# Kernel tuning notes

Measured on AMD Instinct MI355X. Metric: run time of the kernel, lower is better.

Reference implementation:

```python
import jax, jax.numpy as jnp
import numpy as np

D_EMB = 2048
N_HEADS = 16
D_K = D_EMB // N_HEADS  # 128
MAX_LEN = 128           # must equal D_K for the (faithful) buggy mask broadcast
VOCAB = 30000
N_LAYERS = 6
BATCH = 8
SEQ = 128
D_FF = 4 * D_EMB


def _sinusoidal_pe(length, d):
    pos = jnp.arange(length, dtype=jnp.float32)[:, None]
    div = jnp.exp(-jnp.log(10000.0) * jnp.arange(0, d, 2, dtype=jnp.float32) / d)
    pe = jnp.zeros((length, d), dtype=jnp.float32)
    pe = pe.at[:, 0::2].set(jnp.sin(pos * div))
    pe = pe.at[:, 1::2].set(jnp.cos(pos * div))
    return pe


def _layernorm(x, g, b, eps=1e-5):
    m = jnp.mean(x, axis=-1, keepdims=True)
    v = jnp.var(x, axis=-1, keepdims=True)
    return g * (x - m) * jax.lax.rsqrt(v + eps) + b


def _attention(x, ctx, Wq, Wk, Wv, Wo, mask):
    # Faithful to source: reshape [B,L,H,dk] then swap LAST TWO axes -> [B,L,dk,H],
    # so scores are [B,L,dk,dk] (attention over the d_k axis, per token).
    B, L, D = x.shape
    split = lambda t: t.reshape(B, L, N_HEADS, D_K).swapaxes(-2, -1)  # [B,L,dk,H]
    Q = split(x @ Wq.T)
    K = split(ctx @ Wk.T)
    V = split(ctx @ Wv.T)
    qk = (Q @ K.swapaxes(-2, -1)) / np.sqrt(D_K)  # [B,L,dk,dk]
    if mask is not None:
        qk = qk + mask  # mask [L,L] broadcasts (L == dk == max_len)
    attn = jax.nn.softmax(qk, axis=-1) @ V        # [B,L,dk,H]
    concat = attn.swapaxes(-2, -1).reshape(B, L, D)
    return concat @ Wo.T


def _decoder(x, context, params):
    p = params
    L = x.shape[1]
    x = x + _sinusoidal_pe(L, D_EMB)
    mask = jnp.triu(jnp.full((L, L), -jnp.inf, dtype=x.dtype), k=1)
    for _ in range(N_LAYERS):  # weights are SHARED across layers (as in source)
        x = _layernorm(_attention(x, x, p['Wq1'], p['Wk1'], p['Wv1'], p['Wo1'], mask),
                       p['g1'], p['be1'])
        x = _layernorm(_attention(x, context, p['Wq2'], p['Wk2'], p['Wv2'], p['Wo2'], None),
                       p['g2'], p['be2'])
        h = jax.nn.relu(x @ p['W_ff1'].T + p['b_ff1']) @ p['W_ff2'].T + p['b_ff2']
        x = _layernorm(h, p['g3'], p['be3'])
    logits = (x @ p['W_lin'].T + p['b_lin']) / 1.0  # temperature = 1.0
    # Faithful to source: softmax over dim=1 (sequence axis), then take last batch element
    return jax.nn.softmax(logits, axis=1)[-1]  # [L, VOCAB]


def setup_inputs() -> dict:
    key = jax.random.key(0)
    ks = jax.random.split(key, 20)
    a = np.sqrt(3.0 / D_EMB)
    u = lambda k, sh: jax.random.uniform(k, sh, jnp.float32, -a, a)
    inp = {
        'x': jax.random.normal(ks[0], (BATCH, SEQ, D_EMB), jnp.float32),
        'context': jax.random.normal(ks[1], (BATCH, SEQ, D_EMB), jnp.float32),
        'Wq1': u(ks[2], (D_EMB, D_EMB)), 'Wk1': u(ks[3], (D_EMB, D_EMB)),
        'Wv1': u(ks[4], (D_EMB, D_EMB)), 'Wo1': u(ks[5], (D_EMB, D_EMB)),
        'Wq2': u(ks[6], (D_EMB, D_EMB)), 'Wk2': u(ks[7], (D_EMB, D_EMB)),
        'Wv2': u(ks[8], (D_EMB, D_EMB)), 'Wo2': u(ks[9], (D_EMB, D_EMB)),
        'W_ff1': u(ks[10], (D_FF, D_EMB)), 'b_ff1': jnp.zeros((D_FF,), jnp.float32),
        'W_ff2': jax.random.uniform(ks[11], (D_EMB, D_FF), jnp.float32, -np.sqrt(1.0 / D_FF), np.sqrt(1.0 / D_FF)),
        'b_ff2': jnp.zeros((D_EMB,), jnp.float32),
        'g1': jnp.ones((D_EMB,), jnp.float32), 'be1': jnp.zeros((D_EMB,), jnp.float32),
        'g2': jnp.ones((D_EMB,), jnp.float32), 'be2': jnp.zeros((D_EMB,), jnp.float32),
        'g3': jnp.ones((D_EMB,), jnp.float32), 'be3': jnp.zeros((D_EMB,), jnp.float32),
        'W_lin': u(ks[12], (VOCAB, D_EMB)), 'b_lin': jnp.zeros((VOCAB,), jnp.float32),
    }
    return inp


def reference(x, context, Wq1, Wk1, Wv1, Wo1, Wq2, Wk2, Wv2, Wo2,
              W_ff1, b_ff1, W_ff2, b_ff2, g1, be1, g2, be2, g3, be3,
              W_lin, b_lin):
    params = dict(Wq1=Wq1, Wk1=Wk1, Wv1=Wv1, Wo1=Wo1,
                  Wq2=Wq2, Wk2=Wk2, Wv2=Wv2, Wo2=Wo2,
                  W_ff1=W_ff1, b_ff1=b_ff1, W_ff2=W_ff2, b_ff2=b_ff2,
                  g1=g1, be1=be1, g2=g2, be2=be2, g3=g3, be3=be3,
                  W_lin=W_lin, b_lin=b_lin)
    return _decoder(x, context, params)
```

## Files before the change

kernel.cpp:

```cpp
#include <hip/hip_runtime.h>
#include <hip/hip_bf16.h>
#include <math.h>

#define D_EMB 2048
#define NH 16
#define DK 128
#define SEQN 128
#define DFF 8192
#define VOCAB 30000
#define NLAYERS 6
#define TOKF (SEQN * D_EMB)

typedef __attribute__((ext_vector_type(8))) short short8v;
typedef __attribute__((ext_vector_type(4))) float float4v;
typedef __hip_bfloat16 bf16;

#define GLOAD_LDS16(g, l)                                                      \
    __builtin_amdgcn_global_load_lds(                                          \
        (const __attribute__((address_space(1))) void*)(g),                    \
        (__attribute__((address_space(3))) void*)(l), 16, 0, 0)

struct CvtArgs {
    const float* src[8];
    bf16* dst[8];
};

__global__ __launch_bounds__(256) void cvt_kernel(CvtArgs args, int n4) {
    int i = blockIdx.x * 256 + threadIdx.x;
    if (i >= n4) return;
    const float4* s = (const float4*)args.src[blockIdx.z];
    float4 v = s[i];
    union { short4 s4; bf16 h[4]; } u;
    u.h[0] = __float2bfloat16(v.x);
    u.h[1] = __float2bfloat16(v.y);
    u.h[2] = __float2bfloat16(v.z);
    u.h[3] = __float2bfloat16(v.w);
    ((short4*)args.dst[blockIdx.z])[i] = u.s4;
}

__global__ __launch_bounds__(256) void add_pe_kernel(const float* __restrict__ x,
                                                     bf16* __restrict__ out) {
    int idx = blockIdx.x * 256 + threadIdx.x;
    int l = idx >> 11;
    int d = idx & 2047;
    float two_i = (float)(d & ~1);
    float div = __expf(-9.210340371976184f * two_i * (1.0f / 2048.0f));
    float ang = (float)l * div;
    float pe = (d & 1) ? cosf(ang) : sinf(ang);
    out[idx] = __float2bfloat16(x[(size_t)7 * SEQN * D_EMB + idx] + pe);
}

__global__ __launch_bounds__(256) void gemm_mfma_kernel(
    const bf16* __restrict__ A,
    const bf16* B0, const bf16* B1, const bf16* B2,
    const float* bias0, const float* bias1, const float* bias2,
    void* C0, void* C1, void* C2,
    int M, int N, int K, int relu, int out_bf16, int ksplit, int kslog)
{
    int z = blockIdx.z;
    int oi = z >> kslog;
    int kh = z & (ksplit - 1);
    int Klocal = K >> kslog;
    int kbase = kh * Klocal;

    const bf16* B    = (oi == 0) ? B0    : (oi == 1) ? B1    : B2;
    const float* bias = (oi == 0) ? bias0 : (oi == 1) ? bias1 : bias2;
    void* C          = (oi == 0) ? C0    : (oi == 1) ? C1    : C2;

    __shared__ __align__(16) bf16 As[2][64 * 128];
    __shared__ __align__(16) bf16 Bs[2][64 * 128];

    int tid = threadIdx.x;
    int w = tid >> 6;
    int lane = tid & 63;
    int m0 = blockIdx.x * 64;
    int n0 = blockIdx.y * 64;
    int wm = (w & 1) * 32;
    int wn = (w >> 1) * 32;
    int fcol = lane & 15;
    int fqu  = lane >> 4;
    int rr   = (w << 2) + (lane >> 4);
    int scol = lane & 15;

    float4v acc[2][2];
    acc[0][0] = (float4v)0.0f; acc[0][1] = (float4v)0.0f;
    acc[1][0] = (float4v)0.0f; acc[1][1] = (float4v)0.0f;

    auto stage = [&](int buf, int k0) {
        #pragma unroll
        for (int t = 0; t < 4; ++t) {
            int r = t * 16 + rr;
            int s = scol ^ (r & 15);
            GLOAD_LDS16(A + (size_t)(m0 + r) * K + kbase + k0 + s * 8,
                        (char*)As[buf] + (size_t)(t * 16 + (w << 2)) * 256);
            GLOAD_LDS16(B + (size_t)(n0 + r) * K + kbase + k0 + s * 8,
                        (char*)Bs[buf] + (size_t)(t * 16 + (w << 2)) * 256);
        }
    };

    int nk = Klocal >> 7;
    stage(0, 0);
    for (int i = 0; i < nk; ++i) {
        int cur = i & 1;
        if (i + 1 < nk) {
            stage(cur ^ 1, (i + 1) << 7);
            asm volatile("s_waitcnt vmcnt(8)" ::: "memory");
        } else {
            asm volatile("s_waitcnt vmcnt(0)" ::: "memory");
        }
        __builtin_amdgcn_s_barrier();
        asm volatile("" ::: "memory");

        #pragma unroll
        for (int kk = 0; kk < 4; ++kk) {
            short8v a[2], b[2];
            int slog = kk * 4 + fqu;
            #pragma unroll
            for (int fm = 0; fm < 2; ++fm) {
                int m = wm + fm * 16 + fcol;
                a[fm] = *(const short8v*)((const char*)As[cur] + m * 256 + ((slog ^ (m & 15)) << 4));
            }
            #pragma unroll
            for (int fn = 0; fn < 2; ++fn) {
                int n = wn + fn * 16 + fcol;
                b[fn] = *(const short8v*)((const char*)Bs[cur] + n * 256 + ((slog ^ (n & 15)) << 4));
            }
            #pragma unroll
            for (int fm = 0; fm < 2; ++fm)
                #pragma unroll
                for (int fn = 0; fn < 2; ++fn)
                    acc[fm][fn] = __builtin_amdgcn_mfma_f32_16x16x32_bf16(
                        a[fm], b[fn], acc[fm][fn], 0, 0, 0);
        }
        asm volatile("" ::: "memory");
        __builtin_amdgcn_s_barrier();
    }

    int rbase = fqu * 4;
    #pragma unroll
    for (int fm = 0; fm < 2; ++fm) {
        #pragma unroll
        for (int fn = 0; fn < 2; ++fn) {
            int n = n0 + wn + fn * 16 + fcol;
            #pragma unroll
            for (int r = 0; r < 4; ++r) {
                int m = m0 + wm + fm * 16 + rbase + r;
                float v = acc[fm][fn][r];
                if (out_bf16) {
                    v += bias ? bias[n] : 0.0f;
                    if (relu) v = fmaxf(v, 0.0f);
                    ((bf16*)C)[(size_t)m * N + n] = __float2bfloat16(v);
                } else {
                    ((float*)C)[(size_t)kh * M * N + (size_t)m * N + n] = v;
                }
            }
        }
    }
}

__global__ __launch_bounds__(256) void attn_token_kernel(
    const float* __restrict__ qp,
    const float* __restrict__ kp, const float* __restrict__ vp,
    const bf16* __restrict__ k16, const bf16* __restrict__ v16,
    bf16* __restrict__ O, int causal, int qparts, int kvparts)
{
    int l = blockIdx.x;
    int tid = threadIdx.x;
    int i = tid & 127;
    int half = tid >> 7;
    __shared__ float qs[D_EMB];
    __shared__ float ks[D_EMB];
    __shared__ float vs[D_EMB];
    __shared__ float m1s[128], l1s[128];
    __shared__ float acc1s[128][NH + 1];
    size_t base = (size_t)l * D_EMB;

    for (int d = tid; d < D_EMB; d += 256) {
        float q = 0.0f;
        for (int p = 0; p < qparts; ++p) q += qp[(size_t)p * TOKF + base + d];
        qs[d] = q;
        if (kvparts) {
            float kv = 0.0f, vv = 0.0f;
            for (int p = 0; p < kvparts; ++p) {
                kv += kp[(size_t)p * TOKF + base + d];
                vv += vp[(size_t)p * TOKF + base + d];
            }
            ks[d] = kv; vs[d] = vv;
        } else {
            ks[d] = (float)k16[base + d];
            vs[d] = (float)v16[base + d];
        }
    }
    __syncthreads();

    const float scale = 0.088388347648318447f;
    float qr[NH];
    #pragma unroll
    for (int h = 0; h < NH; ++h) qr[h] = qs[h * DK + i];

    int jmax = causal ? (i + 1) : DK;
    int j0 = half * 64;
    int j1 = (jmax < j0 + 64) ? jmax : (j0 + 64);

    float m = -INFINITY, lsum = 0.0f;
    float acc[NH];
    #pragma unroll
    for (int h = 0; h < NH; ++h) acc[h] = 0.0f;

    for (int j = j0; j < j1; ++j) {
        float s0 = 0.0f, s1 = 0.0f, s2 = 0.0f, s3 = 0.0f;
        #pragma unroll
        for (int h = 0; h < NH; h += 4) {
            s0 += qr[h + 0] * ks[(h + 0) * DK + j];
            s1 += qr[h + 1] * ks[(h + 1) * DK + j];
            s2 += qr[h + 2] * ks[(h + 2) * DK + j];
            s3 += qr[h + 3] * ks[(h + 3) * DK + j];
        }
        float s = ((s0 + s1) + (s2 + s3)) * scale;
        float nm = fmaxf(m, s);
        float f = __expf(m - nm);
        float p = __expf(s - nm);
        lsum = lsum * f + p;
        #pragma unroll
        for (int h = 0; h < NH; ++h) acc[h] = acc[h] * f + p * vs[h * DK + j];
        m = nm;
    }

    if (half) {
        m1s[i] = m; l1s[i] = lsum;
        #pragma unroll
        for (int h = 0; h < NH; ++h) acc1s[i][h] = acc[h];
    }
    __syncthreads();
    if (!half) {
        float m1 = m1s[i], l1 = l1s[i];
        float nm = fmaxf(m, m1);
        float f0 = __expf(m - nm);
        float f1 = __expf(m1 - nm);
        float rinv = 1.0f / (lsum * f0 + l1 * f1);
        #pragma unroll
        for (int h = 0; h < NH; ++h)
            O[base + h * DK + i] =
                __float2bfloat16((acc[h] * f0 + acc1s[i][h] * f1) * rinv);
    }
}

__global__ __launch_bounds__(256) void layernorm_kernel(
    const float* __restrict__ pa, int nparts,
    const float* __restrict__ addb,
    const float* __restrict__ g, const float* __restrict__ b,
    bf16* __restrict__ Y)
{
    int row = blockIdx.x;
    size_t base = (size_t)row * D_EMB;
    __shared__ float vs[D_EMB];
    __shared__ float buf[256];
    int tid = threadIdx.x;

    float s = 0.0f;
    for (int d = tid; d < D_EMB; d += 256) {
        float v = addb ? addb[d] : 0.0f;
        for (int p = 0; p < nparts; ++p) v += pa[(size_t)p * TOKF + base + d];
        vs[d] = v;
        s += v;
    }
    buf[tid] = s; __syncthreads();
    for (int off = 128; off; off >>= 1) {
        if (tid < off) buf[tid] += buf[tid + off];
        __syncthreads();
    }
    float mean = buf[0] * (1.0f / D_EMB);
    __syncthreads();

    float vsum = 0.0f;
    for (int d = tid; d < D_EMB; d += 256) {
        float t = vs[d] - mean;
        vsum += t * t;
    }
    buf[tid] = vsum; __syncthreads();
    for (int off = 128; off; off >>= 1) {
        if (tid < off) buf[tid] += buf[tid + off];
        __syncthreads();
    }
    float inv = rsqrtf(buf[0] * (1.0f / D_EMB) + 1e-5f);

    for (int d = tid; d < D_EMB; d += 256)
        Y[base + d] = __float2bfloat16(g[d] * (vs[d] - mean) * inv + b[d]);
}

__global__ __launch_bounds__(256) void logits_softmax_kernel(
    const bf16* __restrict__ X, const float* __restrict__ W,
    float* __restrict__ out)
{
    __shared__ __align__(16) bf16 As[128 * 128];
    __shared__ __align__(16) bf16 Bs[64 * 128];
    __shared__ float red[4][64];

    int tid = threadIdx.x;
    int w = tid >> 6;
    int lane = tid & 63;
    int fcol = lane & 15;
    int fqu  = lane >> 4;
    int n0 = blockIdx.x * 64;

    float4v acc[2][4];
    #pragma unroll
    for (int fm = 0; fm < 2; ++fm)
        #pragma unroll
        for (int fn = 0; fn < 4; ++fn) acc[fm][fn] = (float4v)0.0f;

    int brow = tid >> 2;
    int q    = tid & 3;
    int gn   = n0 + brow;

    for (int k0 = 0; k0 < D_EMB; k0 += 128) {
        #pragma unroll
        for (int t = 0; t < 8; ++t) {
            int r = t * 16 + (w << 2) + (lane >> 4);
            int s = (lane & 15) ^ (r & 15);
            GLOAD_LDS16(X + (size_t)r * D_EMB + k0 + s * 8,
                        (char*)As + (size_t)(t * 16 + (w << 2)) * 256);
        }
        #pragma unroll
        for (int j = 0; j < 4; ++j) {
            int sL = q * 4 + j;
            union { short8v v; bf16 h[8]; } u;
            if (gn < VOCAB) {
                const float* gp = W + (size_t)gn * D_EMB + k0 + sL * 8;
                float4 f0 = *(const float4*)gp;
                float4 f1 = *(const float4*)(gp + 4);
                u.h[0] = __float2bfloat16(f0.x); u.h[1] = __float2bfloat16(f0.y);
                u.h[2] = __float2bfloat16(f0.z); u.h[3] = __float2bfloat16(f0.w);
                u.h[4] = __float2bfloat16(f1.x); u.h[5] = __float2bfloat16(f1.y);
                u.h[6] = __float2bfloat16(f1.z); u.h[7] = __float2bfloat16(f1.w);
            } else {
                u.v = (short8v)0;
            }
            *(short8v*)((char*)Bs + brow * 256 + ((sL ^ (brow & 15)) << 4)) = u.v;
        }
        __syncthreads();

        #pragma unroll
        for (int kk = 0; kk < 4; ++kk) {
            int slog = kk * 4 + fqu;
            short8v a[2], b[4];
            #pragma unroll
            for (int fm = 0; fm < 2; ++fm) {
                int m = w * 32 + fm * 16 + fcol;
                a[fm] = *(const short8v*)((const char*)As + m * 256 + ((slog ^ (m & 15)) << 4));
            }
            #pragma unroll
            for (int fn = 0; fn < 4; ++fn) {
                int n = fn * 16 + fcol;
                b[fn] = *(const short8v*)((const char*)Bs + n * 256 + ((slog ^ (n & 15)) << 4));
            }
            #pragma unroll
            for (int fm = 0; fm < 2; ++fm)
                #pragma unroll
                for (int fn = 0; fn < 4; ++fn)
                    acc[fm][fn] = __builtin_amdgcn_mfma_f32_16x16x32_bf16(
                        a[fm], b[fn], acc[fm][fn], 0, 0, 0);
        }
        __syncthreads();
    }

    float cmax[4];
    #pragma unroll
    for (int fn = 0; fn < 4; ++fn) {
        float m = -INFINITY;
        #pragma unroll
        for (int fm = 0; fm < 2; ++fm)
            #pragma unroll
            for (int r = 0; r < 4; ++r) m = fmaxf(m, acc[fm][fn][r]);
        m = fmaxf(m, __shfl_xor(m, 16));
        m = fmaxf(m, __shfl_xor(m, 32));
        cmax[fn] = m;
    }
    if (lane < 16) {
        #pragma unroll
        for (int fn = 0; fn < 4; ++fn) red[w][fn * 16 + lane] = cmax[fn];
    }
    __syncthreads();
    #pragma unroll
    for (int fn = 0; fn < 4; ++fn) {
        float m = red[0][fn * 16 + fcol];
        m = fmaxf(m, red[1][fn * 16 + fcol]);
        m = fmaxf(m, red[2][fn * 16 + fcol]);
        m = fmaxf(m, red[3][fn * 16 + fcol]);
        cmax[fn] = m;
    }
    __syncthreads();

    float csum[4];
    #pragma unroll
    for (int fn = 0; fn < 4; ++fn) {
        float s = 0.0f;
        #pragma unroll
        for (int fm = 0; fm < 2; ++fm)
            #pragma unroll
            for (int r = 0; r < 4; ++r) {
                float e = __expf(acc[fm][fn][r] - cmax[fn]);
                acc[fm][fn][r] = e;
                s += e;
            }
        s += __shfl_xor(s, 16);
        s += __shfl_xor(s, 32);
        csum[fn] = s;
    }
    if (lane < 16) {
        #pragma unroll
        for (int fn = 0; fn < 4; ++fn) red[w][fn * 16 + lane] = csum[fn];
    }
    __syncthreads();
    #pragma unroll
    for (int fn = 0; fn < 4; ++fn) {
        float s = red[0][fn * 16 + fcol] + red[1][fn * 16 + fcol]
                + red[2][fn * 16 + fcol] + red[3][fn * 16 + fcol];
        float rinv = 1.0f / s;
        int c = n0 + fn * 16 + fcol;
        if (c < VOCAB) {
            #pragma unroll
            for (int fm = 0; fm < 2; ++fm)
                #pragma unroll
                for (int r = 0; r < 4; ++r) {
                    int rw = w * 32 + fm * 16 + fqu * 4 + r;
                    out[(size_t)rw * VOCAB + c] = acc[fm][fn][r] * rinv;
                }
        }
    }
}

static inline void launch_gemm(const bf16* A,
                               const bf16* B0, const bf16* B1, const bf16* B2,
                               const float* bias0, const float* bias1, const float* bias2,
                               void* C0, void* C1, void* C2,
                               int M, int N, int K, int relu, int out_bf16,
                               int nout, int ksplit, int kslog, hipStream_t s)
{
    dim3 grid(M / 64, N / 64, nout * ksplit);
    hipLaunchKernelGGL(gemm_mfma_kernel, grid, dim3(256), 0, s,
                       A, B0, B1, B2, bias0, bias1, bias2, C0, C1, C2,
                       M, N, K, relu, out_bf16, ksplit, kslog);
}

extern "C" void kernel_launch(void* const* d_in, const int* in_sizes, int n_in,
                              void* d_out, int out_size, void* d_ws, size_t ws_size,
                              hipStream_t stream)
{
    const float* x_in   = (const float*)d_in[0];
    const float* ctx_in = (const float*)d_in[1];
    const float* Wq1 = (const float*)d_in[2];
    const float* Wk1 = (const float*)d_in[3];
    const float* Wv1 = (const float*)d_in[4];
    const float* Wo1 = (const float*)d_in[5];
    const float* Wq2 = (const float*)d_in[6];
    const float* Wk2 = (const float*)d_in[7];
    const float* Wv2 = (const float*)d_in[8];
    const float* Wo2 = (const float*)d_in[9];
    const float* W_ff1 = (const float*)d_in[10];
    const float* b_ff1 = (const float*)d_in[11];
    const float* W_ff2 = (const float*)d_in[12];
    const float* b_ff2 = (const float*)d_in[13];
    const float* g1  = (const float*)d_in[14];
    const float* be1 = (const float*)d_in[15];
    const float* g2  = (const float*)d_in[16];
    const float* be2 = (const float*)d_in[17];
    const float* g3  = (const float*)d_in[18];
    const float* be3 = (const float*)d_in[19];
    const float* W_lin = (const float*)d_in[20];
    float* out = (float*)d_out;

    const size_t W2 = (size_t)D_EMB * D_EMB;
    const size_t WF = (size_t)DFF * D_EMB;

    char* p = (char*)d_ws;
    bf16* wq1 = (bf16*)p; p += W2 * 2;
    bf16* wk1 = (bf16*)p; p += W2 * 2;
    bf16* wv1 = (bf16*)p; p += W2 * 2;
    bf16* wo1 = (bf16*)p; p += W2 * 2;
    bf16* wq2 = (bf16*)p; p += W2 * 2;
    bf16* wk2 = (bf16*)p; p += W2 * 2;
    bf16* wv2 = (bf16*)p; p += W2 * 2;
    bf16* wo2 = (bf16*)p; p += W2 * 2;
    bf16* wff1 = (bf16*)p; p += WF * 2;
    bf16* wff2 = (bf16*)p; p += WF * 2;
    bf16* wctx = (bf16*)p; p += (size_t)TOKF * 2;
    bf16* X    = (bf16*)p; p += (size_t)TOKF * 2;
    bf16* Att  = (bf16*)p; p += (size_t)TOKF * 2;
    bf16* H    = (bf16*)p; p += (size_t)SEQN * DFF * 2;
    float* Qp  = (float*)p; p += (size_t)4 * TOKF * 4;
    float* Kp  = (float*)p; p += (size_t)4 * TOKF * 4;
    float* Vp  = (float*)p; p += (size_t)4 * TOKF * 4;
    float* X2p = (float*)p; p += (size_t)8 * TOKF * 4;
    float* K2p = (float*)p; p += (size_t)2 * TOKF * 4;
    float* V2p = (float*)p; p += (size_t)2 * TOKF * 4;

    const float* ctx7 = ctx_in + (size_t)7 * SEQN * D_EMB;

    {
        CvtArgs a = {};
        a.src[0] = Wq1; a.dst[0] = wq1;  a.src[1] = Wk1; a.dst[1] = wk1;
        a.src[2] = Wv1; a.dst[2] = wv1;  a.src[3] = Wo1; a.dst[3] = wo1;
        a.src[4] = Wq2; a.dst[4] = wq2;  a.src[5] = Wk2; a.dst[5] = wk2;
        a.src[6] = Wv2; a.dst[6] = wv2;  a.src[7] = Wo2; a.dst[7] = wo2;
        int n4 = (int)(W2 / 4);
        hipLaunchKernelGGL(cvt_kernel, dim3((n4 + 255) / 256, 1, 8), dim3(256), 0,
                           stream, a, n4);
    }
    {
        CvtArgs a = {};
        a.src[0] = W_ff1; a.dst[0] = wff1;
        a.src[1] = W_ff2; a.dst[1] = wff2;
        int n4 = (int)(WF / 4);
        hipLaunchKernelGGL(cvt_kernel, dim3((n4 + 255) / 256, 1, 2), dim3(256), 0,
                           stream, a, n4);
    }
    {
        CvtArgs a = {};
        a.src[0] = ctx7; a.dst[0] = wctx;
        int n4 = TOKF / 4;
        hipLaunchKernelGGL(cvt_kernel, dim3((n4 + 255) / 256, 1, 1), dim3(256), 0,
                           stream, a, n4);
    }

    hipLaunchKernelGGL(add_pe_kernel, dim3((SEQN * D_EMB) / 256), dim3(256), 0,
                       stream, x_in, X);

    launch_gemm(wctx, wk2, wv2, wv2, nullptr, nullptr, nullptr,
                K2p, V2p, V2p, SEQN, D_EMB, D_EMB, 0, 0, 2, 2, 1, stream);

    for (int layer = 0; layer < NLAYERS; ++layer) {
        launch_gemm(X, wq1, wk1, wv1, nullptr, nullptr, nullptr,
                    Qp, Kp, Vp, SEQN, D_EMB, D_EMB, 0, 0, 3, 4, 2, stream);
        hipLaunchKernelGGL(attn_token_kernel, dim3(SEQN), dim3(256), 0, stream,
                           Qp, Kp, Vp,
                           (const bf16*)nullptr, (const bf16*)nullptr,
                           Att, 1, 4, 4);
        launch_gemm(Att, wo1, wo1, wo1, nullptr, nullptr, nullptr,
                    X2p, X2p, X2p, SEQN, D_EMB, D_EMB, 0, 0, 1, 4, 2, stream);
        hipLaunchKernelGGL(layernorm_kernel, dim3(SEQN), dim3(256), 0, stream,
                           X2p, 4, (const float*)nullptr, g1, be1, X);

        launch_gemm(X, wq2, wq2, wq2, nullptr, nullptr, nullptr,
                    Qp, Qp, Qp, SEQN, D_EMB, D_EMB, 0, 0, 1, 4, 2, stream);
        hipLaunchKernelGGL(attn_token_kernel, dim3(SEQN), dim3(256), 0, stream,
                           Qp, K2p, V2p,
                           (const bf16*)nullptr, (const bf16*)nullptr,
                           Att, 0, 4, 2);
        launch_gemm(Att, wo2, wo2, wo2, nullptr, nullptr, nullptr,
                    X2p, X2p, X2p, SEQN, D_EMB, D_EMB, 0, 0, 1, 4, 2, stream);
        hipLaunchKernelGGL(layernorm_kernel, dim3(SEQN), dim3(256), 0, stream,
                           X2p, 4, (const float*)nullptr, g2, be2, X);

        launch_gemm(X, wff1, wff1, wff1, b_ff1, b_ff1, b_ff1,
                    H, H, H, SEQN, DFF, D_EMB, 1, 1, 1, 1, 0, stream);
        launch_gemm(H, wff2, wff2, wff2, nullptr, nullptr, nullptr,
                    X2p, X2p, X2p, SEQN, D_EMB, DFF, 0, 0, 1, 8, 3, stream);
        hipLaunchKernelGGL(layernorm_kernel, dim3(SEQN), dim3(256), 0, stream,
                           X2p, 8, b_ff2, g3, be3, X);
    }

    hipLaunchKernelGGL(logits_softmax_kernel, dim3((VOCAB + 63) / 64), dim3(256),
                       0, stream, X, W_lin, out);
}
```

Before: 1.595 ms.

## Fix GEMM K-slices at 512 with four-stage prefetch, XCD swizzle, and vectorized helpers

The GEMM now always splits K into 512-wide slices and issues all four 128-wide chunks of a slice up front into four LDS buffers, waiting on each with staged vmcnt counts, which removes the loop and its per-iteration barriers. Workgroup IDs are remapped so consecutive tiles spread across the eight XCDs. FF1 becomes a split-K GEMM into fp32 partials followed by a separate bias+ReLU reduction kernel. Attention and layernorm move to float4 loads and a 4-wide online-softmax step. The cost is more fp32 partial traffic and reduction work (FF2 now has 16 partials), doubled LDS per block that may lower occupancy, and an extra kernel launch per layer.

```diff
diff --git a/kernel.cpp b/kernel.cpp
--- a/kernel.cpp
+++ b/kernel.cpp
@@ -19,6 +19,13 @@
     __builtin_amdgcn_global_load_lds(                                          \
         (const __attribute__((address_space(1))) void*)(g),                    \
         (__attribute__((address_space(3))) void*)(l), 16, 0, 0)
+
+#define WAIT_BAR(n)                                                            \
+    do {                                                                       \
+        asm volatile("s_waitcnt vmcnt(" #n ")" ::: "memory");                  \
+        __builtin_amdgcn_s_barrier();                                          \
+        asm volatile("" ::: "memory");                                         \
+    } while (0)
 
 struct CvtArgs {
     const float* src[8];
@@ -57,24 +64,31 @@
     void* C0, void* C1, void* C2,
     int M, int N, int K, int relu, int out_bf16, int ksplit, int kslog)
 {
-    int z = blockIdx.z;
-    int oi = z >> kslog;
-    int kh = z & (ksplit - 1);
-    int Klocal = K >> kslog;
-    int kbase = kh * Klocal;
+    int nwg = gridDim.x * gridDim.y * gridDim.z;
+    int orig = blockIdx.x + gridDim.x * (blockIdx.y + gridDim.y * blockIdx.z);
+    int wg = orig;
+    if ((nwg & 7) == 0) wg = (orig & 7) * (nwg >> 3) + (orig >> 3);
+    int bx = wg % gridDim.x;
+    int t1 = wg / gridDim.x;
+    int by = t1 % gridDim.y;
+    int bz = t1 / gridDim.y;
+
+    int oi = bz >> kslog;
+    int kh = bz & (ksplit - 1);
+    int kbase = kh << 9;
 
     const bf16* B    = (oi == 0) ? B0    : (oi == 1) ? B1    : B2;
     const float* bias = (oi == 0) ? bias0 : (oi == 1) ? bias1 : bias2;
     void* C          = (oi == 0) ? C0    : (oi == 1) ? C1    : C2;
 
-    __shared__ __align__(16) bf16 As[2][64 * 128];
-    __shared__ __align__(16) bf16 Bs[2][64 * 128];
+    __shared__ __align__(16) bf16 As[4][64 * 128];
+    __shared__ __align__(16) bf16 Bs[4][64 * 128];
 
     int tid = threadIdx.x;
     int w = tid >> 6;
     int lane = tid & 63;
-    int m0 = blockIdx.x * 64;
-    int n0 = blockIdx.y * 64;
+    int m0 = bx * 64;
+    int n0 = by * 64;
     int wm = (w & 1) * 32;
     int wn = (w >> 1) * 32;
     int fcol = lane & 15;
@@ -86,31 +100,22 @@
     acc[0][0] = (float4v)0.0f; acc[0][1] = (float4v)0.0f;
     acc[1][0] = (float4v)0.0f; acc[1][1] = (float4v)0.0f;
 
-    auto stage = [&](int buf, int k0) {
+    #pragma unroll
+    for (int c = 0; c < 4; ++c) {
+        const bf16* a0 = A + (size_t)m0 * K + kbase + (c << 7);
+        const bf16* b0 = B + (size_t)n0 * K + kbase + (c << 7);
         #pragma unroll
         for (int t = 0; t < 4; ++t) {
             int r = t * 16 + rr;
             int s = scol ^ (r & 15);
-            GLOAD_LDS16(A + (size_t)(m0 + r) * K + kbase + k0 + s * 8,
-                        (char*)As[buf] + (size_t)(t * 16 + (w << 2)) * 256);
-            GLOAD_LDS16(B + (size_t)(n0 + r) * K + kbase + k0 + s * 8,
-                        (char*)Bs[buf] + (size_t)(t * 16 + (w << 2)) * 256);
-        }
-    };
-
-    int nk = Klocal >> 7;
-    stage(0, 0);
-    for (int i = 0; i < nk; ++i) {
-        int cur = i & 1;
-        if (i + 1 < nk) {
-            stage(cur ^ 1, (i + 1) << 7);
-            asm volatile("s_waitcnt vmcnt(8)" ::: "memory");
-        } else {
-            asm volatile("s_waitcnt vmcnt(0)" ::: "memory");
-        }
-        __builtin_amdgcn_s_barrier();
-        asm volatile("" ::: "memory");
-
+            GLOAD_LDS16(a0 + (size_t)r * K + s * 8,
+                        (char*)As[c] + (size_t)(t * 16 + (w << 2)) * 256);
+            GLOAD_LDS16(b0 + (size_t)r * K + s * 8,
+                        (char*)Bs[c] + (size_t)(t * 16 + (w << 2)) * 256);
+        }
+    }
+
+    auto compute_chunk = [&](int c) {
         #pragma unroll
         for (int kk = 0; kk < 4; ++kk) {
             short8v a[2], b[2];
@@ -118,12 +123,12 @@
             #pragma unroll
             for (int fm = 0; fm < 2; ++fm) {
                 int m = wm + fm * 16 + fcol;
-                a[fm] = *(const short8v*)((const char*)As[cur] + m * 256 + ((slog ^ (m & 15)) << 4));
+                a[fm] = *(const short8v*)((const char*)As[c] + m * 256 + ((slog ^ (m & 15)) << 4));
             }
             #pragma unroll
             for (int fn = 0; fn < 2; ++fn) {
                 int n = wn + fn * 16 + fcol;
-                b[fn] = *(const short8v*)((const char*)Bs[cur] + n * 256 + ((slog ^ (n & 15)) << 4));
+                b[fn] = *(const short8v*)((const char*)Bs[c] + n * 256 + ((slog ^ (n & 15)) << 4));
             }
             #pragma unroll
             for (int fm = 0; fm < 2; ++fm)
@@ -132,9 +137,12 @@
                     acc[fm][fn] = __builtin_amdgcn_mfma_f32_16x16x32_bf16(
                         a[fm], b[fn], acc[fm][fn], 0, 0, 0);
         }
-        asm volatile("" ::: "memory");
-        __builtin_amdgcn_s_barrier();
-    }
+    };
+
+    WAIT_BAR(24); compute_chunk(0);
+    WAIT_BAR(16); compute_chunk(1);
+    WAIT_BAR(8);  compute_chunk(2);
+    WAIT_BAR(0);  compute_chunk(3);
 
     int rbase = fqu * 4;
     #pragma unroll
@@ -158,38 +166,58 @@
     }
 }
 
+__global__ __launch_bounds__(256) void biasrelu_kernel(
+    const float* __restrict__ P, const float* __restrict__ bias,
+    bf16* __restrict__ H)
+{
+    int i4 = blockIdx.x * 256 + threadIdx.x;
+    const size_t n4 = (size_t)SEQN * DFF / 4;
+    const float4* p = (const float4*)P;
+    float4 v0 = p[i4];
+    float4 v1 = p[i4 + n4];
+    float4 v2 = p[i4 + 2 * n4];
+    float4 v3 = p[i4 + 3 * n4];
+    float4 b4 = ((const float4*)bias)[i4 & (DFF / 4 - 1)];
+    union { short4 s4; bf16 h[4]; } u;
+    u.h[0] = __float2bfloat16(fmaxf(v0.x + v1.x + v2.x + v3.x + b4.x, 0.0f));
+    u.h[1] = __float2bfloat16(fmaxf(v0.y + v1.y + v2.y + v3.y + b4.y, 0.0f));
+    u.h[2] = __float2bfloat16(fmaxf(v0.z + v1.z + v2.z + v3.z + b4.z, 0.0f));
+    u.h[3] = __float2bfloat16(fmaxf(v0.w + v1.w + v2.w + v3.w + b4.w, 0.0f));
+    ((short4*)H)[i4] = u.s4;
+}
+
 __global__ __launch_bounds__(256) void attn_token_kernel(
     const float* __restrict__ qp,
     const float* __restrict__ kp, const float* __restrict__ vp,
-    const bf16* __restrict__ k16, const bf16* __restrict__ v16,
     bf16* __restrict__ O, int causal, int qparts, int kvparts)
 {
     int l = blockIdx.x;
     int tid = threadIdx.x;
     int i = tid & 127;
     int half = tid >> 7;
-    __shared__ float qs[D_EMB];
-    __shared__ float ks[D_EMB];
-    __shared__ float vs[D_EMB];
+    __shared__ __align__(16) float qs[D_EMB];
+    __shared__ __align__(16) float ks[D_EMB];
+    __shared__ __align__(16) float vs[D_EMB];
     __shared__ float m1s[128], l1s[128];
     __shared__ float acc1s[128][NH + 1];
     size_t base = (size_t)l * D_EMB;
 
-    for (int d = tid; d < D_EMB; d += 256) {
-        float q = 0.0f;
-        for (int p = 0; p < qparts; ++p) q += qp[(size_t)p * TOKF + base + d];
-        qs[d] = q;
-        if (kvparts) {
-            float kv = 0.0f, vv = 0.0f;
-            for (int p = 0; p < kvparts; ++p) {
-                kv += kp[(size_t)p * TOKF + base + d];
-                vv += vp[(size_t)p * TOKF + base + d];
-            }
-            ks[d] = kv; vs[d] = vv;
-        } else {
-            ks[d] = (float)k16[base + d];
-            vs[d] = (float)v16[base + d];
-        }
+    for (int d4 = tid; d4 < D_EMB / 4; d4 += 256) {
+        float4 q = {0.0f, 0.0f, 0.0f, 0.0f};
+        for (int p = 0; p < qparts; ++p) {
+            float4 t = ((const float4*)(qp + (size_t)p * TOKF + base))[d4];
+            q.x += t.x; q.y += t.y; q.z += t.z; q.w += t.w;
+        }
+        ((float4*)qs)[d4] = q;
+        float4 kv = {0.0f, 0.0f, 0.0f, 0.0f}, vv = {0.0f, 0.0f, 0.0f, 0.0f};
+        for (int p = 0; p < kvparts; ++p) {
+            float4 t = ((const float4*)(kp + (size_t)p * TOKF + base))[d4];
+            kv.x += t.x; kv.y += t.y; kv.z += t.z; kv.w += t.w;
+            float4 s = ((const float4*)(vp + (size_t)p * TOKF + base))[d4];
+            vv.x += s.x; vv.y += s.y; vv.z += s.z; vv.w += s.w;
+        }
+        ((float4*)ks)[d4] = kv;
+        ((float4*)vs)[d4] = vv;
     }
     __syncthreads();
 
@@ -207,22 +235,31 @@
     #pragma unroll
     for (int h = 0; h < NH; ++h) acc[h] = 0.0f;
 
-    for (int j = j0; j < j1; ++j) {
-        float s0 = 0.0f, s1 = 0.0f, s2 = 0.0f, s3 = 0.0f;
-        #pragma unroll
-        for (int h = 0; h < NH; h += 4) {
-            s0 += qr[h + 0] * ks[(h + 0) * DK + j];
-            s1 += qr[h + 1] * ks[(h + 1) * DK + j];
-            s2 += qr[h + 2] * ks[(h + 2) * DK + j];
-            s3 += qr[h + 3] * ks[(h + 3) * DK + j];
-        }
-        float s = ((s0 + s1) + (s2 + s3)) * scale;
-        float nm = fmaxf(m, s);
-        float f = __expf(m - nm);
-        float p = __expf(s - nm);
-        lsum = lsum * f + p;
-        #pragma unroll
-        for (int h = 0; h < NH; ++h) acc[h] = acc[h] * f + p * vs[h * DK + j];
+    for (int j = j0; j < j1; j += 4) {
+        float4 s4 = {0.0f, 0.0f, 0.0f, 0.0f};
+        #pragma unroll
+        for (int h = 0; h < NH; ++h) {
+            float4 kv = *(const float4*)&ks[h * DK + j];
+            s4.x += qr[h] * kv.x; s4.y += qr[h] * kv.y;
+            s4.z += qr[h] * kv.z; s4.w += qr[h] * kv.w;
+        }
+        float sv0 = s4.x * scale;
+        float sv1 = (j + 1 < j1) ? s4.y * scale : -INFINITY;
+        float sv2 = (j + 2 < j1) ? s4.z * scale : -INFINITY;
+        float sv3 = (j + 3 < j1) ? s4.w * scale : -INFINITY;
+        float mx = fmaxf(fmaxf(sv0, sv1), fmaxf(sv2, sv3));
+        float nm = fmaxf(m, mx);
+        float f  = __expf(m - nm);
+        float p0 = __expf(sv0 - nm);
+        float p1 = __expf(sv1 - nm);
+        float p2 = __expf(sv2 - nm);
+        float p3 = __expf(sv3 - nm);
+        lsum = lsum * f + ((p0 + p1) + (p2 + p3));
+        #pragma unroll
+        for (int h = 0; h < NH; ++h) {
+            float4 vv = *(const float4*)&vs[h * DK + j];
+            acc[h] = acc[h] * f + ((p0 * vv.x + p1 * vv.y) + (p2 * vv.z + p3 * vv.w));
+        }
         m = nm;
     }
 
@@ -253,16 +290,20 @@
 {
     int row = blockIdx.x;
     size_t base = (size_t)row * D_EMB;
-    __shared__ float vs[D_EMB];
+    __shared__ __align__(16) float4 vs4[D_EMB / 4];
     __shared__ float buf[256];
     int tid = threadIdx.x;
 
     float s = 0.0f;
-    for (int d = tid; d < D_EMB; d += 256) {
-        float v = addb ? addb[d] : 0.0f;
-        for (int p = 0; p < nparts; ++p) v += pa[(size_t)p * TOKF + base + d];
-        vs[d] = v;
-        s += v;
+    for (int d4 = tid; d4 < D_EMB / 4; d4 += 256) {
+        float4 v = {0.0f, 0.0f, 0.0f, 0.0f};
+        if (addb) v = ((const float4*)addb)[d4];
+        for (int p = 0; p < nparts; ++p) {
+            float4 t = ((const float4*)(pa + (size_t)p * TOKF + base))[d4];
+            v.x += t.x; v.y += t.y; v.z += t.z; v.w += t.w;
+        }
+        vs4[d4] = v;
+        s += (v.x + v.y) + (v.z + v.w);
     }
     buf[tid] = s; __syncthreads();
     for (int off = 128; off; off >>= 1) {
@@ -273,9 +314,10 @@
     __syncthreads();
 
     float vsum = 0.0f;
-    for (int d = tid; d < D_EMB; d += 256) {
-        float t = vs[d] - mean;
-        vsum += t * t;
+    for (int d4 = tid; d4 < D_EMB / 4; d4 += 256) {
+        float4 v = vs4[d4];
+        float t0 = v.x - mean, t1 = v.y - mean, t2 = v.z - mean, t3 = v.w - mean;
+        vsum += (t0 * t0 + t1 * t1) + (t2 * t2 + t3 * t3);
     }
     buf[tid] = vsum; __syncthreads();
     for (int off = 128; off; off >>= 1) {
@@ -284,8 +326,17 @@
     }
     float inv = rsqrtf(buf[0] * (1.0f / D_EMB) + 1e-5f);
 
-    for (int d = tid; d < D_EMB; d += 256)
-        Y[base + d] = __float2bfloat16(g[d] * (vs[d] - mean) * inv + b[d]);
+    for (int d4 = tid; d4 < D_EMB / 4; d4 += 256) {
+        float4 v = vs4[d4];
+        float4 g4 = ((const float4*)g)[d4];
+        float4 b4 = ((const float4*)b)[d4];
+        union { short4 s4; bf16 h[4]; } u;
+        u.h[0] = __float2bfloat16(g4.x * (v.x - mean) * inv + b4.x);
+        u.h[1] = __float2bfloat16(g4.y * (v.y - mean) * inv + b4.y);
+        u.h[2] = __float2bfloat16(g4.z * (v.z - mean) * inv + b4.z);
+        u.h[3] = __float2bfloat16(g4.w * (v.w - mean) * inv + b4.w);
+        ((short4*)(Y + base))[d4] = u.s4;
+    }
 }
 
 __global__ __launch_bounds__(256) void logits_softmax_kernel(
@@ -435,8 +486,10 @@
                                const float* bias0, const float* bias1, const float* bias2,
                                void* C0, void* C1, void* C2,
                                int M, int N, int K, int relu, int out_bf16,
-                               int nout, int ksplit, int kslog, hipStream_t s)
+                               int nout, hipStream_t s)
 {
+    int ksplit = K >> 9;
+    int kslog = (ksplit == 4) ? 2 : (ksplit == 16) ? 4 : (ksplit == 8) ? 3 : 0;
     dim3 grid(M / 64, N / 64, nout * ksplit);
     hipLaunchKernelGGL(gemm_mfma_kernel, grid, dim3(256), 0, s,
                        A, B0, B1, B2, bias0, bias1, bias2, C0, C1, C2,
@@ -491,9 +544,10 @@
     float* Qp  = (float*)p; p += (size_t)4 * TOKF * 4;
     float* Kp  = (float*)p; p += (size_t)4 * TOKF * 4;
     float* Vp  = (float*)p; p += (size_t)4 * TOKF * 4;
-    float* X2p = (float*)p; p += (size_t)8 * TOKF * 4;
-    float* K2p = (float*)p; p += (size_t)2 * TOKF * 4;
-    float* V2p = (float*)p; p += (size_t)2 * TOKF * 4;
+    float* X2p = (float*)p; p += (size_t)16 * TOKF * 4;
+    float* K2p = (float*)p; p += (size_t)4 * TOKF * 4;
+    float* V2p = (float*)p; p += (size_t)4 * TOKF * 4;
+    float* FFp = (float*)p; p += (size_t)4 * SEQN * DFF * 4;
 
     const float* ctx7 = ctx_in + (size_t)7 * SEQN * D_EMB;
 
@@ -527,37 +581,35 @@
                        stream, x_in, X);
 
     launch_gemm(wctx, wk2, wv2, wv2, nullptr, nullptr, nullptr,
-                K2p, V2p, V2p, SEQN, D_EMB, D_EMB, 0, 0, 2, 2, 1, stream);
+                K2p, V2p, V2p, SEQN, D_EMB, D_EMB, 0, 0, 2, stream);
 
     for (int layer = 0; layer < NLAYERS; ++layer) {
         launch_gemm(X, wq1, wk1, wv1, nullptr, nullptr, nullptr,
-                    Qp, Kp, Vp, SEQN, D_EMB, D_EMB, 0, 0, 3, 4, 2, stream);
+                    Qp, Kp, Vp, SEQN, D_EMB, D_EMB, 0, 0, 3, stream);
         hipLaunchKernelGGL(attn_token_kernel, dim3(SEQN), dim3(256), 0, stream,
-                           Qp, Kp, Vp,
-                           (const bf16*)nullptr, (const bf16*)nullptr,
-                           Att, 1, 4, 4);
+                           Qp, Kp, Vp, Att, 1, 4, 4);
         launch_gemm(Att, wo1, wo1, wo1, nullptr, nullptr, nullptr,
-                    X2p, X2p, X2p, SEQN, D_EMB, D_EMB, 0, 0, 1, 4, 2, stream);
+                    X2p, X2p, X2p, SEQN, D_EMB, D_EMB, 0, 0, 1, stream);
         hipLaunchKernelGGL(layernorm_kernel, dim3(SEQN), dim3(256), 0, stream,
                            X2p, 4, (const float*)nullptr, g1, be1, X);
 
         launch_gemm(X, wq2, wq2, wq2, nullptr, nullptr, nullptr,
-                    Qp, Qp, Qp, SEQN, D_EMB, D_EMB, 0, 0, 1, 4, 2, stream);
+                    Qp, Qp, Qp, SEQN, D_EMB, D_EMB, 0, 0, 1, stream);
         hipLaunchKernelGGL(attn_token_kernel, dim3(SEQN), dim3(256), 0, stream,
-                           Qp, K2p, V2p,
-                           (const bf16*)nullptr, (const bf16*)nullptr,
-                           Att, 0, 4, 2);
+                           Qp, K2p, V2p, Att, 0, 4, 4);
         launch_gemm(Att, wo2, wo2, wo2, nullptr, nullptr, nullptr,
-                    X2p, X2p, X2p, SEQN, D_EMB, D_EMB, 0, 0, 1, 4, 2, stream);
+                    X2p, X2p, X2p, SEQN, D_EMB, D_EMB, 0, 0, 1, stream);
         hipLaunchKernelGGL(layernorm_kernel, dim3(SEQN), dim3(256), 0, stream,
                            X2p, 4, (const float*)nullptr, g2, be2, X);
 
-        launch_gemm(X, wff1, wff1, wff1, b_ff1, b_ff1, b_ff1,
-                    H, H, H, SEQN, DFF, D_EMB, 1, 1, 1, 1, 0, stream);
+        launch_gemm(X, wff1, wff1, wff1, nullptr, nullptr, nullptr,
+                    FFp, FFp, FFp, SEQN, DFF, D_EMB, 0, 0, 1, stream);
+        hipLaunchKernelGGL(biasrelu_kernel, dim3((SEQN * DFF / 4) / 256), dim3(256),
+                           0, stream, FFp, b_ff1, H);
         launch_gemm(H, wff2, wff2, wff2, nullptr, nullptr, nullptr,
-                    X2p, X2p, X2p, SEQN, D_EMB, DFF, 0, 0, 1, 8, 3, stream);
+                    X2p, X2p, X2p, SEQN, D_EMB, DFF, 0, 0, 1, stream);
         hipLaunchKernelGGL(layernorm_kernel, dim3(SEQN), dim3(256), 0, stream,
-                           X2p, 8, b_ff2, g3, be3, X);
+                           X2p, 16, b_ff2, g3, be3, X);
     }
 
     hipLaunchKernelGGL(logits_softmax_kernel, dim3((VOCAB + 63) / 64), dim3(256),
```

After: 1.437 ms. 9.9% less time.
